# Kernel tuning notes

Measured on AMD Instinct MI355X. Metric: run time of the kernel, lower is better.

## Reference

```python
import jax, jax.numpy as jnp
import numpy as np

N_SRC = 50000
N_DST = 50000
N_EDGES = 500000
HIDDEN = 128
HEADS = 8
HEAD_DIM = HIDDEN // HEADS
SCALE = HEAD_DIM ** -0.5


def setup_inputs() -> dict:
    key = jax.random.key(0)
    ks = jax.random.split(key, 12)
    lim = 1.0 / np.sqrt(HIDDEN)
    def lin(k):
        kw, kb = jax.random.split(k)
        W = jax.random.uniform(kw, (HIDDEN, HIDDEN), jnp.float32, -lim, lim)
        b = jax.random.uniform(kb, (HIDDEN,), jnp.float32, -lim, lim)
        return W, b
    Wq, bq = lin(ks[0]); Wk, bk = lin(ks[1]); Wv, bv = lin(ks[2]); Wo, bo = lin(ks[3])
    return {
        "x_src": jax.random.normal(ks[4], (N_SRC, HIDDEN), jnp.float32),
        "x_dst": jax.random.normal(ks[5], (N_DST, HIDDEN), jnp.float32),
        "edge_index": jax.random.randint(ks[6], (2, N_EDGES), 0, N_SRC, jnp.int64),
        "Wq": Wq, "bq": bq, "Wk": Wk, "bk": bk, "Wv": Wv, "bv": bv,
        "Wo": Wo, "bo": bo,
        "edge_bias": jax.random.normal(ks[7], (HEADS,), jnp.float32) * 0.02,
    }


def reference(x_src, x_dst, edge_index, Wq, bq, Wk, bk, Wv, bv, Wo, bo, edge_bias):
    num_dst = x_dst.shape[0]
    # projections (torch Linear: y = x W^T + b), reshape to (N, H, D)
    q = (x_dst @ Wq.T + bq).reshape(num_dst, HEADS, HEAD_DIM)
    k = (x_src @ Wk.T + bk).reshape(-1, HEADS, HEAD_DIM)
    v = (x_src @ Wv.T + bv).reshape(-1, HEADS, HEAD_DIM)
    src_idx, dst_idx = edge_index[0], edge_index[1]
    # per-edge dot-product scores: (E, H)
    scores = (q[dst_idx] * k[src_idx]).sum(-1) * SCALE + edge_bias
    # sparse softmax over edges grouped by destination
    m = jax.ops.segment_max(scores, dst_idx, num_segments=num_dst)  # (N_dst, H)
    e = jnp.exp(scores - m[dst_idx])
    s = jax.ops.segment_sum(e, dst_idx, num_segments=num_dst)  # (N_dst, H)
    w = e / (s[dst_idx] + 1e-8)  # (E, H)
    # scatter-add aggregate weighted values
    out = jax.ops.segment_sum(w[:, :, None] * v[src_idx], dst_idx, num_segments=num_dst)
    out = out.reshape(num_dst, HIDDEN)
    return out @ Wo.T + bo
```

## Files before the change

### kernel.cpp

```cpp
#include <hip/hip_runtime.h>
#include <math.h>

#define HIDDEN 128
#define SCALE 0.25f
#define NB_F 256

typedef __attribute__((ext_vector_type(8))) short short8v;
typedef __attribute__((ext_vector_type(4))) float f32x4;

__device__ __forceinline__ unsigned short f2bf(float f) {
  const unsigned u = __float_as_uint(f);
  const unsigned r = u + 0x7fffu + ((u >> 16) & 1u);
  return (unsigned short)(r >> 16);
}
__device__ __forceinline__ unsigned pack_bf2(float a, float b) {
  unsigned r;
  asm("v_cvt_pk_bf16_f32 %0, %1, %2" : "=v"(r) : "v"(a), "v"(b));
  return r;
}
__device__ __forceinline__ float bflo(unsigned u) { return __uint_as_float(u << 16); }
__device__ __forceinline__ float bfhi(unsigned u) { return __uint_as_float(u & 0xffff0000u); }

__device__ __forceinline__ void gload_lds16(const void* g, void* l) {
  __builtin_amdgcn_global_load_lds(
      (const __attribute__((address_space(1))) unsigned*)g,
      (__attribute__((address_space(3))) unsigned*)l, 16, 0, 0);
}

__global__ __launch_bounds__(256) void init_kernel(
    const float* __restrict__ W0, const float* __restrict__ W1,
    const float* __restrict__ W2, const float* __restrict__ W3,
    unsigned short* __restrict__ Wfrag, int* __restrict__ zero_base, int nzero4)
{
  if (blockIdx.x < 32) {
    const int chunk = blockIdx.x * 256 + threadIdx.x;
    const int m = chunk >> 11;
    const int rem = chunk & 2047;
    const int l = rem & 63;
    const int nkk = rem >> 6;
    const int n = nkk >> 2, kk = nkk & 3;
    const float* W = (m == 0) ? W0 : (m == 1) ? W1 : (m == 2) ? W2 : W3;
    const int row = n * 16 + (l & 15);
    const int k0 = kk * 32 + (l >> 4) * 8;
    const float4 v0 = *(const float4*)&W[row * 128 + k0];
    const float4 v1 = *(const float4*)&W[row * 128 + k0 + 4];
    uint4 o;
    o.x = (unsigned)f2bf(v0.x) | ((unsigned)f2bf(v0.y) << 16);
    o.y = (unsigned)f2bf(v0.z) | ((unsigned)f2bf(v0.w) << 16);
    o.z = (unsigned)f2bf(v1.x) | ((unsigned)f2bf(v1.y) << 16);
    o.w = (unsigned)f2bf(v1.z) | ((unsigned)f2bf(v1.w) << 16);
    *(uint4*)&Wfrag[(size_t)chunk * 8] = o;
  } else {
    const int idx4 = (blockIdx.x - 32) * 256 + threadIdx.x;
    if (idx4 < nzero4)
      *(int4*)&zero_base[idx4 * 4] = make_int4(0, 0, 0, 0);
  }
}

__global__ __launch_bounds__(256, 4) void qkv_count_kernel(
    const float* __restrict__ x_src, const float* __restrict__ x_dst,
    const unsigned short* __restrict__ Wfrag,
    const float* __restrict__ bq, const float* __restrict__ bk,
    const float* __restrict__ bv,
    unsigned short* __restrict__ qb, unsigned short* __restrict__ kvb,
    int Nsrc, int Ndst,
    const int* __restrict__ ei, int E, int* __restrict__ counts)
{
  __shared__ __align__(16) char WsB[32768];
  __shared__ float bias_s[128];
  const int t = threadIdx.x;
  const int bid = blockIdx.x;

  if (bid >= 3 * NB_F) {
    const int e = ((bid - 3 * NB_F) * 256 + t) * 4;
    if (e + 4 <= E) {
      const int4 d = *(const int4*)&ei[E + e];
      atomicAdd(&counts[d.x], 1);
      atomicAdd(&counts[d.y], 1);
      atomicAdd(&counts[d.z], 1);
      atomicAdd(&counts[d.w], 1);
    } else {
      for (int k = e; k < E; ++k) atomicAdd(&counts[ei[E + k]], 1);
    }
    return;
  }

  const int flavor = bid / NB_F, sub = bid % NB_F;
  const float* X; const float* bias; const unsigned short* wbase;
  unsigned short* out; int ostride, ooff, N;
  if (flavor == 0)      { X = x_src; bias = bk; wbase = Wfrag + 16384; out = kvb; ostride = 256; ooff = 0;   N = Nsrc; }
  else if (flavor == 1) { X = x_src; bias = bv; wbase = Wfrag + 32768; out = kvb; ostride = 256; ooff = 128; N = Nsrc; }
  else                  { X = x_dst; bias = bq; wbase = Wfrag;         out = qb;  ostride = 128; ooff = 0;   N = Ndst; }

  #pragma unroll
  for (int it = 0; it < 8; ++it) {
    const int off = (it * 256 + t) * 16;
    gload_lds16((const char*)wbase + off, WsB + off);
  }
  if (t < 128) bias_s[t] = bias[t];
  asm volatile("s_waitcnt vmcnt(0)" ::: "memory");
  __syncthreads();

  const int l = t & 63, w = t >> 6;
  const int r16 = l & 15, g16 = l >> 4;
  const int ntiles = (N + 15) >> 4;
  const int stride = NB_F * 4;
  int tile = sub * 4 + w;
  if (tile >= ntiles) return;

  float4 xv[8];
  {
    const int row = tile * 16 + r16;
    const bool valid = row < N;
    const float* xp = X + (size_t)row * 128 + g16 * 8;
    #pragma unroll
    for (int kk = 0; kk < 4; ++kk) {
      xv[2 * kk]     = valid ? *(const float4*)(xp + kk * 32)     : make_float4(0.f, 0.f, 0.f, 0.f);
      xv[2 * kk + 1] = valid ? *(const float4*)(xp + kk * 32 + 4) : make_float4(0.f, 0.f, 0.f, 0.f);
    }
  }
  for (; tile < ntiles; tile += stride) {
    const int nt = tile + stride;
    short8v a[4];
    #pragma unroll
    for (int kk = 0; kk < 4; ++kk) {
      uint4 u;
      u.x = pack_bf2(xv[2 * kk].x,     xv[2 * kk].y);
      u.y = pack_bf2(xv[2 * kk].z,     xv[2 * kk].w);
      u.z = pack_bf2(xv[2 * kk + 1].x, xv[2 * kk + 1].y);
      u.w = pack_bf2(xv[2 * kk + 1].z, xv[2 * kk + 1].w);
      a[kk] = *(short8v*)&u;
    }
    if (nt < ntiles) {
      const int row = nt * 16 + r16;
      const bool valid = row < N;
      const float* xp = X + (size_t)row * 128 + g16 * 8;
      #pragma unroll
      for (int kk = 0; kk < 4; ++kk) {
        xv[2 * kk]     = valid ? *(const float4*)(xp + kk * 32)     : make_float4(0.f, 0.f, 0.f, 0.f);
        xv[2 * kk + 1] = valid ? *(const float4*)(xp + kk * 32 + 4) : make_float4(0.f, 0.f, 0.f, 0.f);
      }
    }
    f32x4 acc[8];
    #pragma unroll
    for (int n = 0; n < 8; ++n) acc[n] = (f32x4){0.f, 0.f, 0.f, 0.f};
    #pragma unroll
    for (int kk = 0; kk < 4; ++kk) {
      #pragma unroll
      for (int n = 0; n < 8; ++n) {
        const short8v wf = *(const short8v*)&WsB[((n * 4 + kk) * 64 + l) * 16];
        acc[n] = __builtin_amdgcn_mfma_f32_16x16x32_bf16(wf, a[kk], acc[n], 0, 0, 0);
      }
    }
    const int row = tile * 16 + r16;
    if (row < N) {
      unsigned short* orow = out + (size_t)row * ostride + ooff;
      #pragma unroll
      for (int n = 0; n < 8; ++n) {
        const float4 bb = *(const float4*)&bias_s[n * 16 + g16 * 4];
        uint2 o;
        o.x = pack_bf2(acc[n][0] + bb.x, acc[n][1] + bb.y);
        o.y = pack_bf2(acc[n][2] + bb.z, acc[n][3] + bb.w);
        *(uint2*)&orow[n * 16 + g16 * 4] = o;
      }
    }
  }
}

__global__ __launch_bounds__(256, 4) void out_gemm_kernel(
    const unsigned short* __restrict__ agg, const unsigned short* __restrict__ Wfrag_o,
    const float* __restrict__ bo, float* __restrict__ Y, int N)
{
  __shared__ __align__(16) char WsB[32768];
  __shared__ float bias_s[128];
  const int t = threadIdx.x;
  #pragma unroll
  for (int it = 0; it < 8; ++it) {
    const int off = (it * 256 + t) * 16;
    gload_lds16((const char*)Wfrag_o + off, WsB + off);
  }
  if (t < 128) bias_s[t] = bo[t];
  asm volatile("s_waitcnt vmcnt(0)" ::: "memory");
  __syncthreads();

  const int l = t & 63, w = t >> 6;
  const int r16 = l & 15, g16 = l >> 4;
  const int ntiles = (N + 15) >> 4;
  const int stride = NB_F * 4;
  int tile = blockIdx.x * 4 + w;
  if (tile >= ntiles) return;

  uint4 av[4];
  {
    const int row = tile * 16 + r16;
    const bool valid = row < N;
    const unsigned short* ap = agg + (size_t)row * 128 + g16 * 8;
    #pragma unroll
    for (int kk = 0; kk < 4; ++kk)
      av[kk] = valid ? *(const uint4*)(ap + kk * 32) : make_uint4(0, 0, 0, 0);
  }
  for (; tile < ntiles; tile += stride) {
    const int nt = tile + stride;
    short8v a[4];
    #pragma unroll
    for (int kk = 0; kk < 4; ++kk) a[kk] = *(short8v*)&av[kk];
    if (nt < ntiles) {
      const int row = nt * 16 + r16;
      const bool valid = row < N;
      const unsigned short* ap = agg + (size_t)row * 128 + g16 * 8;
      #pragma unroll
      for (int kk = 0; kk < 4; ++kk)
        av[kk] = valid ? *(const uint4*)(ap + kk * 32) : make_uint4(0, 0, 0, 0);
    }
    f32x4 acc[8];
    #pragma unroll
    for (int n = 0; n < 8; ++n) acc[n] = (f32x4){0.f, 0.f, 0.f, 0.f};
    #pragma unroll
    for (int kk = 0; kk < 4; ++kk) {
      #pragma unroll
      for (int n = 0; n < 8; ++n) {
        const short8v wf = *(const short8v*)&WsB[((n * 4 + kk) * 64 + l) * 16];
        acc[n] = __builtin_amdgcn_mfma_f32_16x16x32_bf16(wf, a[kk], acc[n], 0, 0, 0);
      }
    }
    const int row = tile * 16 + r16;
    if (row < N) {
      float* yrow = Y + (size_t)row * 128;
      #pragma unroll
      for (int n = 0; n < 8; ++n) {
        const float4 bb = *(const float4*)&bias_s[n * 16 + g16 * 4];
        *(float4*)&yrow[n * 16 + g16 * 4] =
            make_float4(acc[n][0] + bb.x, acc[n][1] + bb.y, acc[n][2] + bb.z, acc[n][3] + bb.w);
      }
    }
  }
}

__global__ __launch_bounds__(256) void scan_fused_kernel(
    const int* __restrict__ counts, int n, int* __restrict__ bsums,
    int* __restrict__ done, int* __restrict__ offsets)
{
  const int b = blockIdx.x, t = threadIdx.x;
  const int lane = t & 63, wid = t >> 6;
  const int idx = b * 256 + t;
  const int x = (idx < n) ? counts[idx] : 0;
  int v = x;
  #pragma unroll
  for (int off = 1; off < 64; off <<= 1) {
    const int tmp = __shfl_up(v, off);
    if (lane >= off) v += tmp;
  }
  __shared__ int wsum[4];
  __shared__ int base_s;
  if (lane == 63) wsum[wid] = v;
  __syncthreads();
  if (t == 0) {
    bsums[b] = wsum[0] + wsum[1] + wsum[2] + wsum[3];
    __threadfence();
    atomicAdd(done, 1);
    while (atomicAdd(done, 0) < (int)gridDim.x) {}
  }
  __syncthreads();
  __threadfence();
  int pre = (t < b) ? bsums[t] : 0;
  #pragma unroll
  for (int off = 1; off < 64; off <<= 1) pre += __shfl_xor(pre, off);
  __shared__ int pres[4];
  if (lane == 0) pres[wid] = pre;
  __syncthreads();
  if (t == 0) base_s = pres[0] + pres[1] + pres[2] + pres[3];
  __syncthreads();
  int wbase = 0;
  for (int p = 0; p < wid; ++p) wbase += wsum[p];
  if (idx < n) offsets[idx] = base_s + wbase + v - x;
}

__global__ __launch_bounds__(256) void scatter_kernel(
    const int* __restrict__ ei, int E, int* __restrict__ offsets,
    int* __restrict__ csr_src)
{
  const int e = (blockIdx.x * 256 + threadIdx.x) * 4;
  if (e + 4 <= E) {
    const int4 s = *(const int4*)&ei[e];
    const int4 d = *(const int4*)&ei[E + e];
    int p;
    p = atomicAdd(&offsets[d.x], 1); csr_src[p] = s.x;
    p = atomicAdd(&offsets[d.y], 1); csr_src[p] = s.y;
    p = atomicAdd(&offsets[d.z], 1); csr_src[p] = s.z;
    p = atomicAdd(&offsets[d.w], 1); csr_src[p] = s.w;
  } else {
    for (int k = e; k < E; ++k) {
      const int d = ei[E + k];
      const int p = atomicAdd(&offsets[d], 1);
      csr_src[p] = ei[k];
    }
  }
}

__global__ __launch_bounds__(256) void edge_attn_kernel(
    const unsigned short* __restrict__ qb, const unsigned short* __restrict__ kvb,
    const float* __restrict__ eb, const int* __restrict__ offsets,
    const int* __restrict__ counts, const int* __restrict__ csr_src,
    unsigned short* __restrict__ agg, int Ndst)
{
  const int wave = blockIdx.x * 4 + (threadIdx.x >> 6);
  if (wave >= Ndst) return;
  const int lane = threadIdx.x & 63;
  const int eg = lane >> 3, h = lane & 7;

  const uint4 q0 = *(const uint4*)&qb[(size_t)wave * 128 + h * 16];
  const uint4 q1 = *(const uint4*)&qb[(size_t)wave * 128 + h * 16 + 8];
  const float bias = eb[h];
  const int ro = (wave == 0) ? 0 : offsets[wave - 1];
  const int cnt = counts[wave];

  float acc[16];
  #pragma unroll
  for (int j = 0; j < 16; ++j) acc[j] = 0.f;
  float s = 0.f;

  int e = eg;
  bool act = e < cnt;
  int src = act ? csr_src[ro + e] : 0;
  const int iters = (cnt + 7) >> 3;
  for (int it = 0; it < iters; ++it) {
    const size_t base = (size_t)src * 256 + h * 16;
    const uint4 k0 = *(const uint4*)&kvb[base];
    const uint4 k1 = *(const uint4*)&kvb[base + 8];
    const uint4 v0 = *(const uint4*)&kvb[base + 128];
    const uint4 v1 = *(const uint4*)&kvb[base + 136];
    const int e2 = e + 8;
    const bool act2 = e2 < cnt;
    const int src2 = act2 ? csr_src[ro + e2] : 0;

    float p = 0.f;
    p = fmaf(bflo(q0.x), bflo(k0.x), p); p = fmaf(bfhi(q0.x), bfhi(k0.x), p);
    p = fmaf(bflo(q0.y), bflo(k0.y), p); p = fmaf(bfhi(q0.y), bfhi(k0.y), p);
    p = fmaf(bflo(q0.z), bflo(k0.z), p); p = fmaf(bfhi(q0.z), bfhi(k0.z), p);
    p = fmaf(bflo(q0.w), bflo(k0.w), p); p = fmaf(bfhi(q0.w), bfhi(k0.w), p);
    p = fmaf(bflo(q1.x), bflo(k1.x), p); p = fmaf(bfhi(q1.x), bfhi(k1.x), p);
    p = fmaf(bflo(q1.y), bflo(k1.y), p); p = fmaf(bfhi(q1.y), bfhi(k1.y), p);
    p = fmaf(bflo(q1.z), bflo(k1.z), p); p = fmaf(bfhi(q1.z), bfhi(k1.z), p);
    p = fmaf(bflo(q1.w), bflo(k1.w), p); p = fmaf(bfhi(q1.w), bfhi(k1.w), p);

    const float wgt = act ? __expf(fmaf(p, SCALE, bias)) : 0.f;
    s += wgt;
    acc[0]  = fmaf(wgt, bflo(v0.x), acc[0]);  acc[1]  = fmaf(wgt, bfhi(v0.x), acc[1]);
    acc[2]  = fmaf(wgt, bflo(v0.y), acc[2]);  acc[3]  = fmaf(wgt, bfhi(v0.y), acc[3]);
    acc[4]  = fmaf(wgt, bflo(v0.z), acc[4]);  acc[5]  = fmaf(wgt, bfhi(v0.z), acc[5]);
    acc[6]  = fmaf(wgt, bflo(v0.w), acc[6]);  acc[7]  = fmaf(wgt, bfhi(v0.w), acc[7]);
    acc[8]  = fmaf(wgt, bflo(v1.x), acc[8]);  acc[9]  = fmaf(wgt, bfhi(v1.x), acc[9]);
    acc[10] = fmaf(wgt, bflo(v1.y), acc[10]); acc[11] = fmaf(wgt, bfhi(v1.y), acc[11]);
    acc[12] = fmaf(wgt, bflo(v1.z), acc[12]); acc[13] = fmaf(wgt, bfhi(v1.z), acc[13]);
    acc[14] = fmaf(wgt, bflo(v1.w), acc[14]); acc[15] = fmaf(wgt, bfhi(v1.w), acc[15]);
    e = e2; act = act2; src = src2;
  }

  const bool b0 = eg & 1, b1 = (eg >> 1) & 1, b2 = (eg >> 2) & 1;
  float r8[8];
  #pragma unroll
  for (int j = 0; j < 8; ++j) {
    const float keep = b0 ? acc[j + 8] : acc[j];
    const float send = b0 ? acc[j] : acc[j + 8];
    r8[j] = keep + __shfl_xor(send, 8);
  }
  float r4[4];
  #pragma unroll
  for (int j = 0; j < 4; ++j) {
    const float keep = b1 ? r8[j + 4] : r8[j];
    const float send = b1 ? r8[j] : r8[j + 4];
    r4[j] = keep + __shfl_xor(send, 16);
  }
  float r2[2];
  #pragma unroll
  for (int j = 0; j < 2; ++j) {
    const float keep = b2 ? r4[j + 2] : r4[j];
    const float send = b2 ? r4[j] : r4[j + 2];
    r2[j] = keep + __shfl_xor(send, 32);
  }
  s += __shfl_xor(s, 8); s += __shfl_xor(s, 16); s += __shfl_xor(s, 32);
  const float rs = 1.0f / (s + 1e-8f);
  const int col = h * 16 + (b0 ? 8 : 0) + (b1 ? 4 : 0) + (b2 ? 2 : 0);
  *(unsigned*)&agg[(size_t)wave * 128 + col] = pack_bf2(r2[0] * rs, r2[1] * rs);
}

extern "C" void kernel_launch(void* const* d_in, const int* in_sizes, int n_in,
                              void* d_out, int out_size, void* d_ws, size_t ws_size,
                              hipStream_t stream) {
  const float* x_src = (const float*)d_in[0];
  const float* x_dst = (const float*)d_in[1];
  const int*   ei    = (const int*)d_in[2];
  const float* Wq = (const float*)d_in[3];
  const float* bq = (const float*)d_in[4];
  const float* Wk = (const float*)d_in[5];
  const float* bk = (const float*)d_in[6];
  const float* Wv = (const float*)d_in[7];
  const float* bv = (const float*)d_in[8];
  const float* Wo = (const float*)d_in[9];
  const float* bo = (const float*)d_in[10];
  const float* eb = (const float*)d_in[11];

  const int Nsrc = in_sizes[0] / HIDDEN;
  const int Ndst = in_sizes[1] / HIDDEN;
  const int E    = in_sizes[2] / 2;

  char* w = (char*)d_ws;
  unsigned short* qb   = (unsigned short*)w; w += (size_t)Ndst * 128 * 2;
  unsigned short* kvb  = (unsigned short*)w; w += (size_t)Nsrc * 256 * 2;
  unsigned short* aggb = (unsigned short*)w; w += (size_t)Ndst * 128 * 2;
  unsigned short* Wb   = (unsigned short*)w; w += (size_t)4 * 16384 * 2;
  int* counts  = (int*)w; w += (size_t)Ndst * sizeof(int);
  int* done    = (int*)w; w += 64 * sizeof(int);
  int* offsets = (int*)w; w += (size_t)Ndst * sizeof(int);
  int* bsums   = (int*)w; w += 256 * sizeof(int);
  int* csr_src = (int*)w; w += (size_t)E * sizeof(int);

  dim3 blk256(256);
  const int nzero4 = (Ndst + 64 + 3) / 4;
  const int zblocks = (nzero4 + 255) / 256;
  init_kernel<<<32 + zblocks, blk256, 0, stream>>>(Wq, Wk, Wv, Wo, Wb, counts, nzero4);

  const int e4blocks = (E / 4 + 255) / 256;
  qkv_count_kernel<<<3 * NB_F + e4blocks, blk256, 0, stream>>>(
      x_src, x_dst, Wb, bq, bk, bv, qb, kvb, Nsrc, Ndst, ei, E, counts);

  const int nb = (Ndst + 255) / 256;
  scan_fused_kernel<<<nb, blk256, 0, stream>>>(counts, Ndst, bsums, done, offsets);

  scatter_kernel<<<e4blocks, blk256, 0, stream>>>(ei, E, offsets, csr_src);

  const int ablocks = (Ndst + 3) / 4;
  edge_attn_kernel<<<ablocks, blk256, 0, stream>>>(qb, kvb, eb, offsets, counts,
                                                   csr_src, aggb, Ndst);

  out_gemm_kernel<<<NB_F, blk256, 0, stream>>>(aggb, Wb + 49152, bo, (float*)d_out, Ndst);
}
```

Measured before the change: 153.9 us.

## Keep GEMM weight fragments in registers and split output columns across waves

The QKV and output projection kernels stop staging the full bf16 weight matrix in LDS. Each wave now holds a quarter of the weight fragments (4 column blocks × 4 k-steps) in registers, and waves split the work by output column half and row half, or by K versus V. Bias is folded into the accumulator initialisation, the software prefetch of the next tile is dropped, and grid sizes and the count-block ordering change. This removes LDS traffic and the barrier, but each input row is now loaded by two waves and the registers used for weights lower the occupancy target.

```diff
diff --git a/kernel.cpp b/kernel.cpp
--- a/kernel.cpp
+++ b/kernel.cpp
@@ -3,7 +3,9 @@
 
 #define HIDDEN 128
 #define SCALE 0.25f
-#define NB_F 256
+#define NB_KV 1024
+#define NB_Q  512
+#define NB_O  512
 
 typedef __attribute__((ext_vector_type(8))) short short8v;
 typedef __attribute__((ext_vector_type(4))) float f32x4;
@@ -20,12 +22,6 @@
 }
 __device__ __forceinline__ float bflo(unsigned u) { return __uint_as_float(u << 16); }
 __device__ __forceinline__ float bfhi(unsigned u) { return __uint_as_float(u & 0xffff0000u); }
-
-__device__ __forceinline__ void gload_lds16(const void* g, void* l) {
-  __builtin_amdgcn_global_load_lds(
-      (const __attribute__((address_space(1))) unsigned*)g,
-      (__attribute__((address_space(3))) unsigned*)l, 16, 0, 0);
-}
 
 __global__ __launch_bounds__(256) void init_kernel(
     const float* __restrict__ W0, const float* __restrict__ W1,
@@ -57,22 +53,20 @@
   }
 }
 
-__global__ __launch_bounds__(256, 4) void qkv_count_kernel(
+__global__ __launch_bounds__(256, 3) void qkv_count_kernel(
     const float* __restrict__ x_src, const float* __restrict__ x_dst,
     const unsigned short* __restrict__ Wfrag,
     const float* __restrict__ bq, const float* __restrict__ bk,
     const float* __restrict__ bv,
     unsigned short* __restrict__ qb, unsigned short* __restrict__ kvb,
     int Nsrc, int Ndst,
-    const int* __restrict__ ei, int E, int* __restrict__ counts)
-{
-  __shared__ __align__(16) char WsB[32768];
-  __shared__ float bias_s[128];
+    const int* __restrict__ ei, int E, int* __restrict__ counts, int cblocks)
+{
   const int t = threadIdx.x;
-  const int bid = blockIdx.x;
-
-  if (bid >= 3 * NB_F) {
-    const int e = ((bid - 3 * NB_F) * 256 + t) * 4;
+  int bid = blockIdx.x;
+
+  if (bid < cblocks) {
+    const int e = (bid * 256 + t) * 4;
     if (e + 4 <= E) {
       const int4 d = *(const int4*)&ei[E + e];
       atomicAdd(&counts[d.x], 1);
@@ -84,43 +78,52 @@
     }
     return;
   }
-
-  const int flavor = bid / NB_F, sub = bid % NB_F;
-  const float* X; const float* bias; const unsigned short* wbase;
-  unsigned short* out; int ostride, ooff, N;
-  if (flavor == 0)      { X = x_src; bias = bk; wbase = Wfrag + 16384; out = kvb; ostride = 256; ooff = 0;   N = Nsrc; }
-  else if (flavor == 1) { X = x_src; bias = bv; wbase = Wfrag + 32768; out = kvb; ostride = 256; ooff = 128; N = Nsrc; }
-  else                  { X = x_dst; bias = bq; wbase = Wfrag;         out = qb;  ostride = 128; ooff = 0;   N = Ndst; }
-
-  #pragma unroll
-  for (int it = 0; it < 8; ++it) {
-    const int off = (it * 256 + t) * 16;
-    gload_lds16((const char*)wbase + off, WsB + off);
-  }
-  if (t < 128) bias_s[t] = bias[t];
-  asm volatile("s_waitcnt vmcnt(0)" ::: "memory");
-  __syncthreads();
+  bid -= cblocks;
 
   const int l = t & 63, w = t >> 6;
   const int r16 = l & 15, g16 = l >> 4;
-  const int ntiles = (N + 15) >> 4;
-  const int stride = NB_F * 4;
-  int tile = sub * 4 + w;
-  if (tile >= ntiles) return;
-
-  float4 xv[8];
-  {
-    const int row = tile * 16 + r16;
+
+  int cb4, rowmul, rowoff, N, ntiles, stride, tile0, ostride, ooff;
+  const float *X, *bias;
+  const unsigned short* wb;
+  unsigned short* outp;
+  if (bid < NB_KV) {
+    const int isV = w >> 1;
+    cb4 = (w & 1) * 4;
+    wb = Wfrag + (isV ? 32768 : 16384);
+    bias = isV ? bv : bk;
+    X = x_src; outp = kvb; ostride = 256; ooff = isV ? 128 : 0;
+    N = Nsrc; rowmul = 16; rowoff = 0;
+    ntiles = (Nsrc + 15) >> 4; stride = NB_KV; tile0 = bid;
+  } else {
+    cb4 = (w & 1) * 4;
+    wb = Wfrag; bias = bq;
+    X = x_dst; outp = qb; ostride = 128; ooff = 0;
+    N = Ndst; rowmul = 32; rowoff = (w >> 1) * 16;
+    ntiles = (Ndst + 31) >> 5; stride = NB_Q; tile0 = bid - NB_KV;
+  }
+
+  short8v wfr[4][4];
+  #pragma unroll
+  for (int nb = 0; nb < 4; ++nb)
+    #pragma unroll
+    for (int kk = 0; kk < 4; ++kk)
+      wfr[nb][kk] = ((const short8v*)wb)[((cb4 + nb) * 4 + kk) * 64 + l];
+  float4 bb[4];
+  #pragma unroll
+  for (int nb = 0; nb < 4; ++nb)
+    bb[nb] = *(const float4*)&bias[(cb4 + nb) * 16 + g16 * 4];
+
+  for (int tile = tile0; tile < ntiles; tile += stride) {
+    const int row = tile * rowmul + rowoff + r16;
     const bool valid = row < N;
     const float* xp = X + (size_t)row * 128 + g16 * 8;
+    float4 xv[8];
     #pragma unroll
     for (int kk = 0; kk < 4; ++kk) {
       xv[2 * kk]     = valid ? *(const float4*)(xp + kk * 32)     : make_float4(0.f, 0.f, 0.f, 0.f);
       xv[2 * kk + 1] = valid ? *(const float4*)(xp + kk * 32 + 4) : make_float4(0.f, 0.f, 0.f, 0.f);
     }
-  }
-  for (; tile < ntiles; tile += stride) {
-    const int nt = tile + stride;
     short8v a[4];
     #pragma unroll
     for (int kk = 0; kk < 4; ++kk) {
@@ -131,107 +134,75 @@
       u.w = pack_bf2(xv[2 * kk + 1].z, xv[2 * kk + 1].w);
       a[kk] = *(short8v*)&u;
     }
-    if (nt < ntiles) {
-      const int row = nt * 16 + r16;
-      const bool valid = row < N;
-      const float* xp = X + (size_t)row * 128 + g16 * 8;
+    f32x4 acc[4];
+    #pragma unroll
+    for (int nb = 0; nb < 4; ++nb)
+      acc[nb] = (f32x4){bb[nb].x, bb[nb].y, bb[nb].z, bb[nb].w};
+    #pragma unroll
+    for (int kk = 0; kk < 4; ++kk)
       #pragma unroll
-      for (int kk = 0; kk < 4; ++kk) {
-        xv[2 * kk]     = valid ? *(const float4*)(xp + kk * 32)     : make_float4(0.f, 0.f, 0.f, 0.f);
-        xv[2 * kk + 1] = valid ? *(const float4*)(xp + kk * 32 + 4) : make_float4(0.f, 0.f, 0.f, 0.f);
+      for (int nb = 0; nb < 4; ++nb)
+        acc[nb] = __builtin_amdgcn_mfma_f32_16x16x32_bf16(wfr[nb][kk], a[kk], acc[nb], 0, 0, 0);
+    if (valid) {
+      unsigned short* orow = outp + (size_t)row * ostride + ooff;
+      #pragma unroll
+      for (int nb = 0; nb < 4; ++nb) {
+        uint2 o;
+        o.x = pack_bf2(acc[nb][0], acc[nb][1]);
+        o.y = pack_bf2(acc[nb][2], acc[nb][3]);
+        *(uint2*)&orow[(cb4 + nb) * 16 + g16 * 4] = o;
       }
     }
-    f32x4 acc[8];
-    #pragma unroll
-    for (int n = 0; n < 8; ++n) acc[n] = (f32x4){0.f, 0.f, 0.f, 0.f};
-    #pragma unroll
-    for (int kk = 0; kk < 4; ++kk) {
-      #pragma unroll
-      for (int n = 0; n < 8; ++n) {
-        const short8v wf = *(const short8v*)&WsB[((n * 4 + kk) * 64 + l) * 16];
-        acc[n] = __builtin_amdgcn_mfma_f32_16x16x32_bf16(wf, a[kk], acc[n], 0, 0, 0);
-      }
-    }
-    const int row = tile * 16 + r16;
-    if (row < N) {
-      unsigned short* orow = out + (size_t)row * ostride + ooff;
-      #pragma unroll
-      for (int n = 0; n < 8; ++n) {
-        const float4 bb = *(const float4*)&bias_s[n * 16 + g16 * 4];
-        uint2 o;
-        o.x = pack_bf2(acc[n][0] + bb.x, acc[n][1] + bb.y);
-        o.y = pack_bf2(acc[n][2] + bb.z, acc[n][3] + bb.w);
-        *(uint2*)&orow[n * 16 + g16 * 4] = o;
-      }
-    }
-  }
-}
-
-__global__ __launch_bounds__(256, 4) void out_gemm_kernel(
+  }
+}
+
+__global__ __launch_bounds__(256, 3) void out_gemm_kernel(
     const unsigned short* __restrict__ agg, const unsigned short* __restrict__ Wfrag_o,
     const float* __restrict__ bo, float* __restrict__ Y, int N)
 {
-  __shared__ __align__(16) char WsB[32768];
-  __shared__ float bias_s[128];
   const int t = threadIdx.x;
-  #pragma unroll
-  for (int it = 0; it < 8; ++it) {
-    const int off = (it * 256 + t) * 16;
-    gload_lds16((const char*)Wfrag_o + off, WsB + off);
-  }
-  if (t < 128) bias_s[t] = bo[t];
-  asm volatile("s_waitcnt vmcnt(0)" ::: "memory");
-  __syncthreads();
-
   const int l = t & 63, w = t >> 6;
   const int r16 = l & 15, g16 = l >> 4;
-  const int ntiles = (N + 15) >> 4;
-  const int stride = NB_F * 4;
-  int tile = blockIdx.x * 4 + w;
-  if (tile >= ntiles) return;
-
-  uint4 av[4];
-  {
-    const int row = tile * 16 + r16;
+  const int cb4 = (w & 1) * 4;
+  const int rowoff = (w >> 1) * 16;
+  const int ntiles = (N + 31) >> 5;
+
+  short8v wfr[4][4];
+  #pragma unroll
+  for (int nb = 0; nb < 4; ++nb)
+    #pragma unroll
+    for (int kk = 0; kk < 4; ++kk)
+      wfr[nb][kk] = ((const short8v*)Wfrag_o)[((cb4 + nb) * 4 + kk) * 64 + l];
+  float4 bb[4];
+  #pragma unroll
+  for (int nb = 0; nb < 4; ++nb)
+    bb[nb] = *(const float4*)&bo[(cb4 + nb) * 16 + g16 * 4];
+
+  for (int tile = blockIdx.x; tile < ntiles; tile += NB_O) {
+    const int row = tile * 32 + rowoff + r16;
     const bool valid = row < N;
     const unsigned short* ap = agg + (size_t)row * 128 + g16 * 8;
+    uint4 av[4];
     #pragma unroll
     for (int kk = 0; kk < 4; ++kk)
       av[kk] = valid ? *(const uint4*)(ap + kk * 32) : make_uint4(0, 0, 0, 0);
-  }
-  for (; tile < ntiles; tile += stride) {
-    const int nt = tile + stride;
-    short8v a[4];
-    #pragma unroll
-    for (int kk = 0; kk < 4; ++kk) a[kk] = *(short8v*)&av[kk];
-    if (nt < ntiles) {
-      const int row = nt * 16 + r16;
-      const bool valid = row < N;
-      const unsigned short* ap = agg + (size_t)row * 128 + g16 * 8;
+    f32x4 acc[4];
+    #pragma unroll
+    for (int nb = 0; nb < 4; ++nb)
+      acc[nb] = (f32x4){bb[nb].x, bb[nb].y, bb[nb].z, bb[nb].w};
+    #pragma unroll
+    for (int kk = 0; kk < 4; ++kk) {
+      const short8v a = *(const short8v*)&av[kk];
       #pragma unroll
-      for (int kk = 0; kk < 4; ++kk)
-        av[kk] = valid ? *(const uint4*)(ap + kk * 32) : make_uint4(0, 0, 0, 0);
-    }
-    f32x4 acc[8];
-    #pragma unroll
-    for (int n = 0; n < 8; ++n) acc[n] = (f32x4){0.f, 0.f, 0.f, 0.f};
-    #pragma unroll
-    for (int kk = 0; kk < 4; ++kk) {
-      #pragma unroll
-      for (int n = 0; n < 8; ++n) {
-        const short8v wf = *(const short8v*)&WsB[((n * 4 + kk) * 64 + l) * 16];
-        acc[n] = __builtin_amdgcn_mfma_f32_16x16x32_bf16(wf, a[kk], acc[n], 0, 0, 0);
-      }
-    }
-    const int row = tile * 16 + r16;
-    if (row < N) {
+      for (int nb = 0; nb < 4; ++nb)
+        acc[nb] = __builtin_amdgcn_mfma_f32_16x16x32_bf16(wfr[nb][kk], a, acc[nb], 0, 0, 0);
+    }
+    if (valid) {
       float* yrow = Y + (size_t)row * 128;
       #pragma unroll
-      for (int n = 0; n < 8; ++n) {
-        const float4 bb = *(const float4*)&bias_s[n * 16 + g16 * 4];
-        *(float4*)&yrow[n * 16 + g16 * 4] =
-            make_float4(acc[n][0] + bb.x, acc[n][1] + bb.y, acc[n][2] + bb.z, acc[n][3] + bb.w);
-      }
+      for (int nb = 0; nb < 4; ++nb)
+        *(float4*)&yrow[(cb4 + nb) * 16 + g16 * 4] =
+            make_float4(acc[nb][0], acc[nb][1], acc[nb][2], acc[nb][3]);
     }
   }
 }
@@ -421,8 +392,8 @@
   init_kernel<<<32 + zblocks, blk256, 0, stream>>>(Wq, Wk, Wv, Wo, Wb, counts, nzero4);
 
   const int e4blocks = (E / 4 + 255) / 256;
-  qkv_count_kernel<<<3 * NB_F + e4blocks, blk256, 0, stream>>>(
-      x_src, x_dst, Wb, bq, bk, bv, qb, kvb, Nsrc, Ndst, ei, E, counts);
+  qkv_count_kernel<<<e4blocks + NB_KV + NB_Q, blk256, 0, stream>>>(
+      x_src, x_dst, Wb, bq, bk, bv, qb, kvb, Nsrc, Ndst, ei, E, counts, e4blocks);
 
   const int nb = (Ndst + 255) / 256;
   scan_fused_kernel<<<nb, blk256, 0, stream>>>(counts, Ndst, bsums, done, offsets);
@@ -433,5 +404,5 @@
   edge_attn_kernel<<<ablocks, blk256, 0, stream>>>(qb, kvb, eb, offsets, counts,
                                                    csr_src, aggb, Ndst);
 
-  out_gemm_kernel<<<NB_F, blk256, 0, stream>>>(aggb, Wb + 49152, bo, (float*)d_out, Ndst);
-}
+  out_gemm_kernel<<<NB_O, blk256, 0, stream>>>(aggb, Wb + 49152, bo, (float*)d_out, Ndst);
+}
```

After: 155.9 us. About the same (+1.3%).

## Fuse scan with scatter, reorder count blocks first, deepen edge-attn prefetch

Applied to the files above, without the earlier changes.

The scan and CSR scatter are merged into one kernel: scan blocks publish their offsets and then signal a second counter, and every block spin-waits on that counter before scattering. This removes one kernel launch boundary. In the QKV kernel the edge-counting blocks now come first in the grid so their atomics start earlier. In the attention kernel the K/V row for the next edge is loaded one iteration ahead, with the source index two ahead, to hide gather latency at the cost of more registers. The grid-wide spin-wait depends on all scan blocks being resident at the same time, which adds a deadlock risk.

```diff
diff --git a/kernel.cpp b/kernel.cpp
--- a/kernel.cpp
+++ b/kernel.cpp
@@ -64,15 +64,15 @@
     const float* __restrict__ bv,
     unsigned short* __restrict__ qb, unsigned short* __restrict__ kvb,
     int Nsrc, int Ndst,
-    const int* __restrict__ ei, int E, int* __restrict__ counts)
+    const int* __restrict__ ei, int E, int* __restrict__ counts, int cblocks)
 {
   __shared__ __align__(16) char WsB[32768];
   __shared__ float bias_s[128];
   const int t = threadIdx.x;
-  const int bid = blockIdx.x;
-
-  if (bid >= 3 * NB_F) {
-    const int e = ((bid - 3 * NB_F) * 256 + t) * 4;
+  int bid = blockIdx.x;
+
+  if (bid < cblocks) {
+    const int e = (bid * 256 + t) * 4;
     if (e + 4 <= E) {
       const int4 d = *(const int4*)&ei[E + e];
       atomicAdd(&counts[d.x], 1);
@@ -84,6 +84,7 @@
     }
     return;
   }
+  bid -= cblocks;
 
   const int flavor = bid / NB_F, sub = bid % NB_F;
   const float* X; const float* bias; const unsigned short* wbase;
@@ -236,50 +237,55 @@
   }
 }
 
-__global__ __launch_bounds__(256) void scan_fused_kernel(
+__global__ __launch_bounds__(256) void scan_scatter_kernel(
     const int* __restrict__ counts, int n, int* __restrict__ bsums,
-    int* __restrict__ done, int* __restrict__ offsets)
+    int* __restrict__ done, int* __restrict__ offsets, int nb_scan,
+    const int* __restrict__ ei, int E, int* __restrict__ csr_src)
 {
   const int b = blockIdx.x, t = threadIdx.x;
-  const int lane = t & 63, wid = t >> 6;
-  const int idx = b * 256 + t;
-  const int x = (idx < n) ? counts[idx] : 0;
-  int v = x;
-  #pragma unroll
-  for (int off = 1; off < 64; off <<= 1) {
-    const int tmp = __shfl_up(v, off);
-    if (lane >= off) v += tmp;
-  }
-  __shared__ int wsum[4];
-  __shared__ int base_s;
-  if (lane == 63) wsum[wid] = v;
-  __syncthreads();
+  if (b < nb_scan) {
+    const int lane = t & 63, wid = t >> 6;
+    const int idx = b * 256 + t;
+    const int x = (idx < n) ? counts[idx] : 0;
+    int v = x;
+    #pragma unroll
+    for (int off = 1; off < 64; off <<= 1) {
+      const int tmp = __shfl_up(v, off);
+      if (lane >= off) v += tmp;
+    }
+    __shared__ int wsum[4];
+    __shared__ int base_s;
+    if (lane == 63) wsum[wid] = v;
+    __syncthreads();
+    if (t == 0) {
+      bsums[b] = wsum[0] + wsum[1] + wsum[2] + wsum[3];
+      __threadfence();
+      atomicAdd(&done[0], 1);
+      while (atomicAdd(&done[0], 0) < nb_scan) {}
+    }
+    __syncthreads();
+    __threadfence();
+    int pre = (t < b) ? bsums[t] : 0;
+    #pragma unroll
+    for (int off = 1; off < 64; off <<= 1) pre += __shfl_xor(pre, off);
+    __shared__ int pres[4];
+    if (lane == 0) pres[wid] = pre;
+    __syncthreads();
+    if (t == 0) base_s = pres[0] + pres[1] + pres[2] + pres[3];
+    __syncthreads();
+    int wbase = 0;
+    for (int p = 0; p < wid; ++p) wbase += wsum[p];
+    if (idx < n) offsets[idx] = base_s + wbase + v - x;
+    __threadfence();
+    __syncthreads();
+    if (t == 0) atomicAdd(&done[1], 1);
+  }
   if (t == 0) {
-    bsums[b] = wsum[0] + wsum[1] + wsum[2] + wsum[3];
-    __threadfence();
-    atomicAdd(done, 1);
-    while (atomicAdd(done, 0) < (int)gridDim.x) {}
+    while (atomicAdd(&done[1], 0) < nb_scan) {}
   }
   __syncthreads();
   __threadfence();
-  int pre = (t < b) ? bsums[t] : 0;
-  #pragma unroll
-  for (int off = 1; off < 64; off <<= 1) pre += __shfl_xor(pre, off);
-  __shared__ int pres[4];
-  if (lane == 0) pres[wid] = pre;
-  __syncthreads();
-  if (t == 0) base_s = pres[0] + pres[1] + pres[2] + pres[3];
-  __syncthreads();
-  int wbase = 0;
-  for (int p = 0; p < wid; ++p) wbase += wsum[p];
-  if (idx < n) offsets[idx] = base_s + wbase + v - x;
-}
-
-__global__ __launch_bounds__(256) void scatter_kernel(
-    const int* __restrict__ ei, int E, int* __restrict__ offsets,
-    int* __restrict__ csr_src)
-{
-  const int e = (blockIdx.x * 256 + threadIdx.x) * 4;
+  const int e = (b * 256 + t) * 4;
   if (e + 4 <= E) {
     const int4 s = *(const int4*)&ei[e];
     const int4 d = *(const int4*)&ei[E + e];
@@ -289,7 +295,7 @@
     p = atomicAdd(&offsets[d.z], 1); csr_src[p] = s.z;
     p = atomicAdd(&offsets[d.w], 1); csr_src[p] = s.w;
   } else {
-    for (int k = e; k < E; ++k) {
+    for (int k = e; k < E && k >= 0; ++k) {
       const int d = ei[E + k];
       const int p = atomicAdd(&offsets[d], 1);
       csr_src[p] = ei[k];
@@ -319,41 +325,52 @@
   for (int j = 0; j < 16; ++j) acc[j] = 0.f;
   float s = 0.f;
 
-  int e = eg;
-  bool act = e < cnt;
-  int src = act ? csr_src[ro + e] : 0;
   const int iters = (cnt + 7) >> 3;
+  int eA = eg;
+  bool actA = eA < cnt;
+  int srcA = actA ? csr_src[ro + eA] : 0;
+  size_t baseA = (size_t)srcA * 256 + h * 16;
+  uint4 kA0 = *(const uint4*)&kvb[baseA];
+  uint4 kA1 = *(const uint4*)&kvb[baseA + 8];
+  uint4 vA0 = *(const uint4*)&kvb[baseA + 128];
+  uint4 vA1 = *(const uint4*)&kvb[baseA + 136];
+  int eB = eA + 8;
+  bool actB = eB < cnt;
+  int srcB = actB ? csr_src[ro + eB] : 0;
+
   for (int it = 0; it < iters; ++it) {
-    const size_t base = (size_t)src * 256 + h * 16;
-    const uint4 k0 = *(const uint4*)&kvb[base];
-    const uint4 k1 = *(const uint4*)&kvb[base + 8];
-    const uint4 v0 = *(const uint4*)&kvb[base + 128];
-    const uint4 v1 = *(const uint4*)&kvb[base + 136];
-    const int e2 = e + 8;
-    const bool act2 = e2 < cnt;
-    const int src2 = act2 ? csr_src[ro + e2] : 0;
+    const size_t baseB = (size_t)srcB * 256 + h * 16;
+    const uint4 kB0 = *(const uint4*)&kvb[baseB];
+    const uint4 kB1 = *(const uint4*)&kvb[baseB + 8];
+    const uint4 vB0 = *(const uint4*)&kvb[baseB + 128];
+    const uint4 vB1 = *(const uint4*)&kvb[baseB + 136];
+    const int eC = eB + 8;
+    const bool actC = eC < cnt;
+    const int srcC = actC ? csr_src[ro + eC] : 0;
 
     float p = 0.f;
-    p = fmaf(bflo(q0.x), bflo(k0.x), p); p = fmaf(bfhi(q0.x), bfhi(k0.x), p);
-    p = fmaf(bflo(q0.y), bflo(k0.y), p); p = fmaf(bfhi(q0.y), bfhi(k0.y), p);
-    p = fmaf(bflo(q0.z), bflo(k0.z), p); p = fmaf(bfhi(q0.z), bfhi(k0.z), p);
-    p = fmaf(bflo(q0.w), bflo(k0.w), p); p = fmaf(bfhi(q0.w), bfhi(k0.w), p);
-    p = fmaf(bflo(q1.x), bflo(k1.x), p); p = fmaf(bfhi(q1.x), bfhi(k1.x), p);
-    p = fmaf(bflo(q1.y), bflo(k1.y), p); p = fmaf(bfhi(q1.y), bfhi(k1.y), p);
-    p = fmaf(bflo(q1.z), bflo(k1.z), p); p = fmaf(bfhi(q1.z), bfhi(k1.z), p);
-    p = fmaf(bflo(q1.w), bflo(k1.w), p); p = fmaf(bfhi(q1.w), bfhi(k1.w), p);
-
-    const float wgt = act ? __expf(fmaf(p, SCALE, bias)) : 0.f;
+    p = fmaf(bflo(q0.x), bflo(kA0.x), p); p = fmaf(bfhi(q0.x), bfhi(kA0.x), p);
+    p = fmaf(bflo(q0.y), bflo(kA0.y), p); p = fmaf(bfhi(q0.y), bfhi(kA0.y), p);
+    p = fmaf(bflo(q0.z), bflo(kA0.z), p); p = fmaf(bfhi(q0.z), bfhi(kA0.z), p);
+    p = fmaf(bflo(q0.w), bflo(kA0.w), p); p = fmaf(bfhi(q0.w), bfhi(kA0.w), p);
+    p = fmaf(bflo(q1.x), bflo(kA1.x), p); p = fmaf(bfhi(q1.x), bfhi(kA1.x), p);
+    p = fmaf(bflo(q1.y), bflo(kA1.y), p); p = fmaf(bfhi(q1.y), bfhi(kA1.y), p);
+    p = fmaf(bflo(q1.z), bflo(kA1.z), p); p = fmaf(bfhi(q1.z), bfhi(kA1.z), p);
+    p = fmaf(bflo(q1.w), bflo(kA1.w), p); p = fmaf(bfhi(q1.w), bfhi(kA1.w), p);
+
+    const float wgt = actA ? __expf(fmaf(p, SCALE, bias)) : 0.f;
     s += wgt;
-    acc[0]  = fmaf(wgt, bflo(v0.x), acc[0]);  acc[1]  = fmaf(wgt, bfhi(v0.x), acc[1]);
-    acc[2]  = fmaf(wgt, bflo(v0.y), acc[2]);  acc[3]  = fmaf(wgt, bfhi(v0.y), acc[3]);
-    acc[4]  = fmaf(wgt, bflo(v0.z), acc[4]);  acc[5]  = fmaf(wgt, bfhi(v0.z), acc[5]);
-    acc[6]  = fmaf(wgt, bflo(v0.w), acc[6]);  acc[7]  = fmaf(wgt, bfhi(v0.w), acc[7]);
-    acc[8]  = fmaf(wgt, bflo(v1.x), acc[8]);  acc[9]  = fmaf(wgt, bfhi(v1.x), acc[9]);
-    acc[10] = fmaf(wgt, bflo(v1.y), acc[10]); acc[11] = fmaf(wgt, bfhi(v1.y), acc[11]);
-    acc[12] = fmaf(wgt, bflo(v1.z), acc[12]); acc[13] = fmaf(wgt, bfhi(v1.z), acc[13]);
-    acc[14] = fmaf(wgt, bflo(v1.w), acc[14]); acc[15] = fmaf(wgt, bfhi(v1.w), acc[15]);
-    e = e2; act = act2; src = src2;
+    acc[0]  = fmaf(wgt, bflo(vA0.x), acc[0]);  acc[1]  = fmaf(wgt, bfhi(vA0.x), acc[1]);
+    acc[2]  = fmaf(wgt, bflo(vA0.y), acc[2]);  acc[3]  = fmaf(wgt, bfhi(vA0.y), acc[3]);
+    acc[4]  = fmaf(wgt, bflo(vA0.z), acc[4]);  acc[5]  = fmaf(wgt, bfhi(vA0.z), acc[5]);
+    acc[6]  = fmaf(wgt, bflo(vA0.w), acc[6]);  acc[7]  = fmaf(wgt, bfhi(vA0.w), acc[7]);
+    acc[8]  = fmaf(wgt, bflo(vA1.x), acc[8]);  acc[9]  = fmaf(wgt, bfhi(vA1.x), acc[9]);
+    acc[10] = fmaf(wgt, bflo(vA1.y), acc[10]); acc[11] = fmaf(wgt, bfhi(vA1.y), acc[11]);
+    acc[12] = fmaf(wgt, bflo(vA1.z), acc[12]); acc[13] = fmaf(wgt, bfhi(vA1.z), acc[13]);
+    acc[14] = fmaf(wgt, bflo(vA1.w), acc[14]); acc[15] = fmaf(wgt, bfhi(vA1.w), acc[15]);
+
+    kA0 = kB0; kA1 = kB1; vA0 = vB0; vA1 = vB1;
+    actA = actB; actB = actC; srcB = srcC; eB = eC;
   }
 
   const bool b0 = eg & 1, b1 = (eg >> 1) & 1, b2 = (eg >> 2) & 1;
@@ -421,13 +438,13 @@
   init_kernel<<<32 + zblocks, blk256, 0, stream>>>(Wq, Wk, Wv, Wo, Wb, counts, nzero4);
 
   const int e4blocks = (E / 4 + 255) / 256;
-  qkv_count_kernel<<<3 * NB_F + e4blocks, blk256, 0, stream>>>(
-      x_src, x_dst, Wb, bq, bk, bv, qb, kvb, Nsrc, Ndst, ei, E, counts);
+  qkv_count_kernel<<<e4blocks + 3 * NB_F, blk256, 0, stream>>>(
+      x_src, x_dst, Wb, bq, bk, bv, qb, kvb, Nsrc, Ndst, ei, E, counts, e4blocks);
 
   const int nb = (Ndst + 255) / 256;
-  scan_fused_kernel<<<nb, blk256, 0, stream>>>(counts, Ndst, bsums, done, offsets);
-
-  scatter_kernel<<<e4blocks, blk256, 0, stream>>>(ei, E, offsets, csr_src);
+  const int sblocks = (e4blocks > nb) ? e4blocks : nb;
+  scan_scatter_kernel<<<sblocks, blk256, 0, stream>>>(
+      counts, Ndst, bsums, done, offsets, nb, ei, E, csr_src);
 
   const int ablocks = (Ndst + 3) / 4;
   edge_attn_kernel<<<ablocks, blk256, 0, stream>>>(qb, kvb, eb, offsets, counts,
```

After: 228.0 us. 1.48x slower.
